# Optimization experiments

Hardware: AMD Instinct MI355X
Metric: run time of the kernel (lower is better)

Reference implementation:

```python
import jax, jax.numpy as jnp
import numpy as np

B, T, C = 2, 2048, 1024
H, HS, RD = 16, 64, 64
KV_R, Q_R = 256, 384


def _rope_tables(T, dim):
    # standard RoPE angle tables, shape [T, dim]
    half = dim // 2
    inv_freq = 1.0 / (10000.0 ** (np.arange(0, half, dtype=np.float32) / half))
    t = np.arange(T, dtype=np.float32)
    ang = np.outer(t, inv_freq)  # [T, half]
    ang = np.concatenate([ang, ang], axis=-1)  # [T, dim]
    return jnp.asarray(np.cos(ang)), jnp.asarray(np.sin(ang))


def setup_inputs() -> dict:
    key = jax.random.key(0)
    ks = jax.random.split(key, 8)
    cos, sin = _rope_tables(T, RD)
    s = lambda fan_in: 1.0 / np.sqrt(fan_in)
    return {
        "x": jax.random.normal(ks[0], (B, T, C), jnp.float32),
        "cos": cos,
        "sin": sin,
        "W_kv_down": jax.random.normal(ks[1], (C, KV_R), jnp.float32) * s(C),
        "W_kv_up": jax.random.normal(ks[2], (KV_R, H * HS), jnp.float32) * s(KV_R),
        "W_k_rope": jax.random.normal(ks[3], (KV_R, H * RD), jnp.float32) * s(KV_R),
        "W_q_down": jax.random.normal(ks[4], (C, Q_R), jnp.float32) * s(C),
        "W_q_up": jax.random.normal(ks[5], (Q_R, H * HS), jnp.float32) * s(Q_R),
        "W_q_rope": jax.random.normal(ks[6], (Q_R, H * RD), jnp.float32) * s(Q_R),
        "W_out": jax.random.normal(ks[7], (H * HS, C), jnp.float32) * s(H * HS),
    }


def _apply_rope(x, cos, sin):
    # x: [B,H,T,D]; cos/sin: [T,D] broadcast
    d = x.shape[-1]
    x1, x2 = x[..., : d // 2], x[..., d // 2 :]
    rotated = jnp.concatenate([-x2, x1], axis=-1)
    return x * cos + rotated * sin


def reference(x, cos, sin, W_kv_down, W_kv_up, W_k_rope, W_q_down, W_q_up, W_q_rope, W_out):
    Bx, Tx, Cx = x.shape
    to_heads = lambda z, d: jnp.swapaxes(z.reshape(Bx, Tx, H, d), 1, 2)  # [B,H,T,d]

    latent_kv = x @ W_kv_down                      # [B,T,KV_R]
    kv_up = latent_kv @ W_kv_up                    # [B,T,H*HS]
    v = to_heads(kv_up, HS)
    k_content = to_heads(kv_up, HS)                # same projection used for k and v
    k_rope = _apply_rope(to_heads(latent_kv @ W_k_rope, RD), cos[:Tx], sin[:Tx])

    latent_q = x @ W_q_down                        # [B,T,Q_R]
    q_content = to_heads(latent_q @ W_q_up, HS)
    q_rope = _apply_rope(to_heads(latent_q @ W_q_rope, RD), cos[:Tx], sin[:Tx])

    q = jnp.concatenate([q_content, q_rope], axis=-1)  # [B,H,T,HS+RD]
    k = jnp.concatenate([k_content, k_rope], axis=-1)

    att = jnp.einsum("bhqd,bhkd->bhqk", q, k) * (HS ** -0.5)
    causal = jnp.tril(jnp.ones((Tx, Tx), bool))
    att = jnp.where(causal, att, -jnp.inf)
    att = jax.nn.softmax(att, axis=-1)             # dropout is eval-mode identity
    y = jnp.einsum("bhqk,bhkd->bhqd", att, v)      # [B,H,T,HS]
    y = jnp.swapaxes(y, 1, 2).reshape(Bx, Tx, H * HS)
    return y @ W_out
```

## Files before the change

### kernel.cpp

```cpp
#include <hip/hip_runtime.h>
#include <stdint.h>

typedef unsigned short u16;
typedef __bf16 bf16x8 __attribute__((ext_vector_type(8)));
typedef float f32x4 __attribute__((ext_vector_type(4)));

#define B_ 2
#define T_ 2048

__device__ __forceinline__ u16 f2b(float f) {
  unsigned u = __float_as_uint(f);
  u += 0x7fffu + ((u >> 16) & 1u);
  return (u16)(u >> 16);
}
__device__ __forceinline__ unsigned cvt_pk(float lo, float hi) {
  unsigned r;
  asm("v_cvt_pk_bf16_f32 %0, %1, %2" : "=v"(r) : "v"(lo), "v"(hi));
  return r;
}
__device__ __forceinline__ float ex2(float x) {
  float r;
  asm("v_exp_f32 %0, %1" : "=v"(r) : "v"(x));
  return r;
}

using gu32 = __attribute__((address_space(1))) const unsigned int;
using lu32 = __attribute__((address_space(3))) unsigned int;
__device__ __forceinline__ void gl_lds16(const u16* g, u16* l) {
  __builtin_amdgcn_global_load_lds((gu32*)g, (lu32*)l, 16, 0, 0);
}

struct TJob { const float* src; u16* dst; int K, N, ldt, row_off, blk0; };
struct TJobs { TJob j[7]; };

__global__ __launch_bounds__(256) void prep_kernel(const float* __restrict__ x,
                                                   u16* __restrict__ xb, TJobs jobs) {
  int bid = blockIdx.x;
  int tid = threadIdx.x;
  if (bid < 4096) {
    int i = (bid * 256 + tid) * 4;
    float4 v = *reinterpret_cast<const float4*>(x + i);
    union { u16 h[4]; unsigned long long ll; } pk;
    pk.h[0] = f2b(v.x); pk.h[1] = f2b(v.y); pk.h[2] = f2b(v.z); pk.h[3] = f2b(v.w);
    *reinterpret_cast<unsigned long long*>(xb + i) = pk.ll;
    return;
  }
  bid -= 4096;
  __shared__ float tile[32][33];
  int ji = 0;
  #pragma unroll
  for (int i = 6; i > 0; --i)
    if (bid >= jobs.j[i].blk0) { ji = i; break; }
  const TJob jb = jobs.j[ji];
  int local = bid - jb.blk0;
  int nb = jb.N >> 5;
  int n0 = (local % nb) * 32, k0 = (local / nb) * 32;
  int cx = tid & 31, ry = tid >> 5;
  #pragma unroll
  for (int i = 0; i < 4; i++)
    tile[ry + i * 8][cx] = jb.src[(size_t)(k0 + ry + i * 8) * jb.N + n0 + cx];
  __syncthreads();
  #pragma unroll
  for (int i = 0; i < 4; i++)
    jb.dst[(size_t)(jb.row_off + n0 + ry + i * 8) * jb.ldt + k0 + cx] =
        f2b(tile[cx][ry + i * 8]);
}

struct GJob { const u16* A; const u16* Bt; void* C; int lda, ldb, ldc, K, mode; };

__global__ __launch_bounds__(512) void gemm_bt8(GJob j0, GJob j1, int split,
                                                const float* __restrict__ cosT,
                                                const float* __restrict__ sinT) {
  __shared__ u16 As[2][128 * 64];
  __shared__ u16 Bs[2][128 * 64];
  const bool first = (int)blockIdx.x < split;
  const GJob jb = first ? j0 : j1;
  const int bx = blockIdx.x - (first ? 0 : split);
  const int tid = threadIdx.x;
  const int wave = tid >> 6, lane = tid & 63;
  const int wr = wave >> 1, wc = wave & 1;
  const int l15 = lane & 15, l4 = lane >> 4;
  const int m0 = blockIdx.y * 128, n0 = bx * 128;
  const int srow = lane >> 3;
  const int scol = ((lane & 7) ^ srow) * 8;

  f32x4 acc[2][4];
  const f32x4 fzero = {0.f, 0.f, 0.f, 0.f};
  #pragma unroll
  for (int m = 0; m < 2; m++)
    #pragma unroll
    for (int n = 0; n < 4; n++)
      acc[m][n] = fzero;

  const u16* gA = jb.A  + (size_t)(m0 + wave * 16 + srow) * jb.lda + scol;
  const u16* gB = jb.Bt + (size_t)(n0 + wave * 16 + srow) * jb.ldb + scol;

  auto stage = [&](int buf, int k0) {
    gl_lds16(gA + k0,                      &As[buf][(wave * 16) * 64]);
    gl_lds16(gA + (size_t)8 * jb.lda + k0, &As[buf][(wave * 16 + 8) * 64]);
    gl_lds16(gB + k0,                      &Bs[buf][(wave * 16) * 64]);
    gl_lds16(gB + (size_t)8 * jb.ldb + k0, &Bs[buf][(wave * 16 + 8) * 64]);
  };

  stage(0, 0);
  int buf = 0;
  const int K = jb.K;
  for (int k0 = 0; k0 < K; k0 += 64) {
    asm volatile("s_waitcnt vmcnt(0)" ::: "memory");
    __builtin_amdgcn_s_barrier();
    if (k0 + 64 < K) stage(buf ^ 1, k0 + 64);
    bf16x8 af[2][2], bfr[4][2];
    #pragma unroll
    for (int m = 0; m < 2; m++) {
      const int row = wr * 32 + m * 16 + l15;
      const int xm = (row & 7) * 8;
      af[m][0] = *reinterpret_cast<const bf16x8*>(&As[buf][row * 64 + ((l4 * 8) ^ xm)]);
      af[m][1] = *reinterpret_cast<const bf16x8*>(&As[buf][row * 64 + ((32 + l4 * 8) ^ xm)]);
    }
    #pragma unroll
    for (int n = 0; n < 4; n++) {
      const int row = wc * 64 + n * 16 + l15;
      const int xm = (row & 7) * 8;
      bfr[n][0] = *reinterpret_cast<const bf16x8*>(&Bs[buf][row * 64 + ((l4 * 8) ^ xm)]);
      bfr[n][1] = *reinterpret_cast<const bf16x8*>(&Bs[buf][row * 64 + ((32 + l4 * 8) ^ xm)]);
    }
    #pragma unroll
    for (int m = 0; m < 2; m++)
      #pragma unroll
      for (int n = 0; n < 4; n++) {
        acc[m][n] = __builtin_amdgcn_mfma_f32_16x16x32_bf16(af[m][0], bfr[n][0], acc[m][n], 0, 0, 0);
        acc[m][n] = __builtin_amdgcn_mfma_f32_16x16x32_bf16(af[m][1], bfr[n][1], acc[m][n], 0, 0, 0);
      }
    buf ^= 1;
  }

  const int row_base = m0 + wr * 32 + l4 * 4;
  const int col_base = n0 + wc * 64 + l15;
  const int mode = jb.mode;
  const int ldc = jb.ldc;

  if (mode == 1) {
    float* Cf = (float*)jb.C;
    #pragma unroll
    for (int m = 0; m < 2; m++)
      #pragma unroll
      for (int n = 0; n < 4; n++)
        #pragma unroll
        for (int r = 0; r < 4; r++)
          Cf[(size_t)(row_base + m * 16 + r) * ldc + col_base + n * 16] = acc[m][n][r];
    return;
  }

  if (mode >= 2 && (n0 + wc * 64) >= 1024) {
    #pragma unroll
    for (int m = 0; m < 2; m++)
      #pragma unroll
      for (int r = 0; r < 4; r++) {
        int t = (row_base + m * 16 + r) & (T_ - 1);
        const float* cp = cosT + t * 64 + l15;
        const float* sp = sinT + t * 64 + l15;
        float c0 = cp[0], c16 = cp[16], c32 = cp[32], c48 = cp[48];
        float s0 = sp[0], s16 = sp[16], s32 = sp[32], s48 = sp[48];
        float x0 = acc[m][0][r], x1 = acc[m][1][r];
        float x2 = acc[m][2][r], x3 = acc[m][3][r];
        acc[m][0][r] = x0 * c0 - x2 * s0;
        acc[m][1][r] = x1 * c16 - x3 * s16;
        acc[m][2][r] = x2 * c32 + x0 * s32;
        acc[m][3][r] = x3 * c48 + x1 * s48;
      }
  }

  u16* Cb = (u16*)jb.C;
  #pragma unroll
  for (int m = 0; m < 2; m++)
    #pragma unroll
    for (int n = 0; n < 4; n++)
      #pragma unroll
      for (int r = 0; r < 4; r++)
        Cb[(size_t)(row_base + m * 16 + r) * ldc + col_base + n * 16] = f2b(acc[m][n][r]);
}

__global__ __launch_bounds__(256) void vtrans_kernel(const u16* __restrict__ kvo,
                                                     u16* __restrict__ vt) {
  __shared__ u16 tile[64][72];
  const int tid = threadIdx.x;
  const int cb = blockIdx.x * 64;
  const int rb = blockIdx.y * 64;
  const int b = rb >> 11, t0 = rb & 2047;
  const int rr = tid >> 3;
  const int c8 = (tid & 7) * 8;
  #pragma unroll
  for (int i = 0; i < 2; i++) {
    int r = i * 32 + rr;
    uint4 v = *reinterpret_cast<const uint4*>(kvo + (size_t)(rb + r) * 2048 + cb + c8);
    *reinterpret_cast<uint4*>(&tile[r][c8]) = v;
  }
  __syncthreads();
  #pragma unroll
  for (int i = 0; i < 2; i++) {
    int c = i * 32 + rr;
    int r8 = c8;
    union { u16 h[8]; uint4 v; } pk;
    #pragma unroll
    for (int j = 0; j < 8; j++) pk.h[j] = tile[r8 + j][c];
    *reinterpret_cast<uint4*>(&vt[(size_t)(b * 1024 + cb + c) * 2048 + t0 + r8]) = pk.v;
  }
}

__global__ __launch_bounds__(512) void attn_kernel(const u16* __restrict__ qo,
                                                   const u16* __restrict__ kvo,
                                                   const u16* __restrict__ vtg,
                                                   u16* __restrict__ yb) {
  __shared__ u16 K_lds[2][64 * 128];
  __shared__ u16 V_lds[2][64 * 64];
  __shared__ u16 P_lds[8][16][72];
  const int tid = threadIdx.x;
  const int wave = tid >> 6, lane = tid & 63;
  const int l15 = lane & 15, l4 = lane >> 4;
  const int bid = blockIdx.x;
  const int bh = bid & 31;
  const int qi = 15 - (bid >> 5);
  const int b = bh >> 4, h = bh & 15;
  const int q0 = qi * 128;
  const int qrow = q0 + wave * 16 + l15;

  const u16* qb = qo + (size_t)(b * T_ + qrow) * 2048 + h * 64;
  bf16x8 qf[4];
  qf[0] = *reinterpret_cast<const bf16x8*>(qb + l4 * 8);
  qf[1] = *reinterpret_cast<const bf16x8*>(qb + 32 + l4 * 8);
  qf[2] = *reinterpret_cast<const bf16x8*>(qb + 1024 + l4 * 8);
  qf[3] = *reinterpret_cast<const bf16x8*>(qb + 1056 + l4 * 8);

  const u16* Kbase = kvo + (size_t)(b * T_) * 2048 + h * 64;
  const u16* Vbase = vtg + (size_t)(b * 1024 + h * 64) * 2048;

  const int krow_i = lane >> 4;
  const int kc2 = (lane & 15) * 16;
  const int vrow_i = lane >> 3;
  const int vc2 = (lane & 7) * 16;

  auto stage = [&](int buf, int kv0) {
    #pragma unroll
    for (int j = 0; j < 2; j++) {
      int row = wave * 8 + j * 4 + krow_i;
      int c2x = kc2 ^ ((row & 7) << 4);
      int cu = c2x >> 1;
      const u16* src = Kbase + (size_t)(kv0 + row) * 2048 + (cu < 64 ? cu : 960 + cu);
      gl_lds16(src, &K_lds[buf][(wave * 8 + j * 4) * 128]);
    }
    {
      int row = wave * 8 + vrow_i;
      int c2x = vc2 ^ ((row & 7) << 4);
      const u16* src = Vbase + (size_t)row * 2048 + kv0 + (c2x >> 1);
      gl_lds16(src, &V_lds[buf][(wave * 8) * 64]);
    }
  };

  const f32x4 fzero = {0.f, 0.f, 0.f, 0.f};
  f32x4 oT[4];
  #pragma unroll
  for (int f = 0; f < 4; f++) oT[f] = fzero;
  float m_run = -1e30f, l_run = 0.f;

  const float SCALE2 = 0.125f * 1.44269504f;
  const int nt = qi * 2 + 2;
  const int t_diag = qi * 2 + (wave >> 2);

  stage(0, 0);
  int buf = 0;

  for (int t = 0; t < nt; t++) {
    const int kv0 = t * 64;
    asm volatile("s_waitcnt vmcnt(0)" ::: "memory");
    __builtin_amdgcn_s_barrier();
    if (t + 1 < nt) stage(buf ^ 1, kv0 + 64);

    if (t <= t_diag) {
      const char* Kb = (const char*)&K_lds[buf][0];
      const char* Vb = (const char*)&V_lds[buf][0];

      f32x4 sT[4];
      #pragma unroll
      for (int c = 0; c < 4; c++) sT[c] = fzero;
      #pragma unroll
      for (int c = 0; c < 4; c++) {
        const int krow = c * 16 + l15;
        const int kxm = (krow & 7) << 4;
        #pragma unroll
        for (int s = 0; s < 4; s++) {
          bf16x8 kf = *reinterpret_cast<const bf16x8*>(
              Kb + krow * 256 + ((s * 64 + l4 * 16) ^ kxm));
          sT[c] = __builtin_amdgcn_mfma_f32_16x16x32_bf16(kf, qf[s], sT[c], 0, 0, 0);
        }
      }

      const bool diag = (t == t_diag);
      float p[4][4];
      float mx = -1e30f;
      #pragma unroll
      for (int c = 0; c < 4; c++)
        #pragma unroll
        for (int r = 0; r < 4; r++) {
          float s = sT[c][r] * SCALE2;
          if (diag) {
            int kv = kv0 + c * 16 + l4 * 4 + r;
            if (kv > qrow) s = -1e30f;
          }
          p[c][r] = s;
          mx = fmaxf(mx, s);
        }
      mx = fmaxf(mx, __shfl_xor(mx, 16));
      mx = fmaxf(mx, __shfl_xor(mx, 32));
      if (__any(mx > m_run + 11.5f)) {
        float m_new = fmaxf(m_run, mx);
        float corr = ex2(m_run - m_new);
        l_run *= corr;
        #pragma unroll
        for (int f = 0; f < 4; f++) oT[f] *= corr;
        m_run = m_new;
      }
      float rsum = 0.f;
      #pragma unroll
      for (int c = 0; c < 4; c++)
        #pragma unroll
        for (int r = 0; r < 4; r++) {
          float pe = ex2(p[c][r] - m_run);
          p[c][r] = pe;
          rsum += pe;
        }
      rsum += __shfl_xor(rsum, 16);
      rsum += __shfl_xor(rsum, 32);
      l_run += rsum;

      #pragma unroll
      for (int c = 0; c < 4; c++) {
        uint2 pk2;
        pk2.x = cvt_pk(p[c][0], p[c][1]);
        pk2.y = cvt_pk(p[c][2], p[c][3]);
        *reinterpret_cast<uint2*>(&P_lds[wave][l15][c * 16 + l4 * 4]) = pk2;
      }
      bf16x8 pb0 = *reinterpret_cast<const bf16x8*>(&P_lds[wave][l15][l4 * 8]);
      bf16x8 pb1 = *reinterpret_cast<const bf16x8*>(&P_lds[wave][l15][32 + l4 * 8]);

      #pragma unroll
      for (int f = 0; f < 4; f++) {
        const int vrow = f * 16 + l15;
        const int vxm = (vrow & 7) << 4;
        bf16x8 v0 = *reinterpret_cast<const bf16x8*>(Vb + vrow * 128 + ((l4 * 16) ^ vxm));
        bf16x8 v1 = *reinterpret_cast<const bf16x8*>(Vb + vrow * 128 + ((64 + l4 * 16) ^ vxm));
        oT[f] = __builtin_amdgcn_mfma_f32_16x16x32_bf16(v0, pb0, oT[f], 0, 0, 0);
        oT[f] = __builtin_amdgcn_mfma_f32_16x16x32_bf16(v1, pb1, oT[f], 0, 0, 0);
      }
    }

    buf ^= 1;
  }

  const float inv = 1.f / l_run;
  #pragma unroll
  for (int f = 0; f < 4; f++) {
    uint2 pk2;
    pk2.x = cvt_pk(oT[f][0] * inv, oT[f][1] * inv);
    pk2.y = cvt_pk(oT[f][2] * inv, oT[f][3] * inv);
    *reinterpret_cast<uint2*>(
        &yb[(size_t)(b * T_ + qrow) * 1024 + h * 64 + f * 16 + l4 * 4]) = pk2;
  }
}

extern "C" void kernel_launch(void* const* d_in, const int* in_sizes, int n_in,
                              void* d_out, int out_size, void* d_ws, size_t ws_size,
                              hipStream_t stream) {
  const float* x         = (const float*)d_in[0];
  const float* cosT      = (const float*)d_in[1];
  const float* sinT      = (const float*)d_in[2];
  const float* W_kv_down = (const float*)d_in[3];
  const float* W_kv_up   = (const float*)d_in[4];
  const float* W_k_rope  = (const float*)d_in[5];
  const float* W_q_down  = (const float*)d_in[6];
  const float* W_q_up    = (const float*)d_in[7];
  const float* W_q_rope  = (const float*)d_in[8];
  const float* W_out     = (const float*)d_in[9];
  float* out = (float*)d_out;
  char* ws = (char*)d_ws;

  u16* xb    = (u16*)(ws + 0);
  u16* lat   = (u16*)(ws + 8388608);
  u16* WdT   = (u16*)(ws + 13631488);
  u16* WkvT  = (u16*)(ws + 14942208);
  u16* WqT   = (u16*)(ws + 15990784);
  u16* WoutT = (u16*)(ws + 17563648);
  u16* kvo   = (u16*)(ws + 19660800);
  u16* qo    = (u16*)(ws + 36438016);
  u16* VT    = (u16*)(ws + 53215232);
  u16* yb    = (u16*)(ws + 0);

  TJobs jobs;
  jobs.j[0] = {W_kv_down, WdT,   1024, 256,  1024, 0,    0};
  jobs.j[1] = {W_q_down,  WdT,   1024, 384,  1024, 256,  256};
  jobs.j[2] = {W_kv_up,   WkvT,  256,  1024, 256,  0,    640};
  jobs.j[3] = {W_k_rope,  WkvT,  256,  1024, 256,  1024, 896};
  jobs.j[4] = {W_q_up,    WqT,   384,  1024, 384,  0,    1152};
  jobs.j[5] = {W_q_rope,  WqT,   384,  1024, 384,  1024, 1536};
  jobs.j[6] = {W_out,     WoutT, 1024, 1024, 1024, 0,    1920};
  prep_kernel<<<7040, 256, 0, stream>>>(x, xb, jobs);

  GJob g1 = {xb, WdT, lat, 1024, 1024, 640, 1024, 0};
  gemm_bt8<<<dim3(5, 32), 512, 0, stream>>>(g1, g1, 5, nullptr, nullptr);

  GJob g2 = {lat,       WkvT, kvo, 640, 256, 2048, 256, 2};
  GJob g3 = {lat + 256, WqT,  qo,  640, 384, 2048, 384, 3};
  gemm_bt8<<<dim3(32, 32), 512, 0, stream>>>(g2, g3, 16, cosT, sinT);

  vtrans_kernel<<<dim3(16, 64), 256, 0, stream>>>(kvo, VT);

  attn_kernel<<<512, 512, 0, stream>>>(qo, kvo, VT, yb);

  GJob g4 = {yb, WoutT, out, 1024, 1024, 1024, 1024, 1};
  gemm_bt8<<<dim3(8, 32), 512, 0, stream>>>(g4, g4, 8, nullptr, nullptr);
}
```

Before: 215.7 us.

## Feed P to PV MFMA from registers and use 64-row tiles for small GEMMs

In attention, the softmax probabilities are packed to bf16 and fed directly as the B operand of 16x16x16 bf16 MFMAs through inline asm. This drops the per-wave P round trip through shared memory, since the accumulator layout of QK^T matches the operand layout of the K=16 MFMA. V is now read as four 8-byte fragments instead of two 16-byte ones. Separately, the GEMM becomes a template over M-tile size, and the down-projection and output GEMMs use 64-row tiles to double the block count for better CU occupancy. The cost is more MFMA instructions of half the K depth and less reuse per block.

```diff
diff --git a/kernel.cpp b/kernel.cpp
--- a/kernel.cpp
+++ b/kernel.cpp
@@ -22,6 +22,10 @@
   float r;
   asm("v_exp_f32 %0, %1" : "=v"(r) : "v"(x));
   return r;
+}
+__device__ __forceinline__ void mfma16(f32x4& acc, uint2 a, uint2 b) {
+  asm volatile("v_mfma_f32_16x16x16_bf16 %0, %1, %2, %0"
+               : "+v"(acc) : "v"(a), "v"(b));
 }
 
 using gu32 = __attribute__((address_space(1))) const unsigned int;
@@ -68,10 +72,12 @@
 
 struct GJob { const u16* A; const u16* Bt; void* C; int lda, ldb, ldc, K, mode; };
 
-__global__ __launch_bounds__(512) void gemm_bt8(GJob j0, GJob j1, int split,
-                                                const float* __restrict__ cosT,
-                                                const float* __restrict__ sinT) {
-  __shared__ u16 As[2][128 * 64];
+template<int ID, int MT>
+__global__ __launch_bounds__(512) void gemm_k(GJob j0, GJob j1, int split,
+                                              const float* __restrict__ cosT,
+                                              const float* __restrict__ sinT) {
+  constexpr int MR = MT / 64;
+  __shared__ u16 As[2][MT * 64];
   __shared__ u16 Bs[2][128 * 64];
   const bool first = (int)blockIdx.x < split;
   const GJob jb = first ? j0 : j1;
@@ -80,24 +86,28 @@
   const int wave = tid >> 6, lane = tid & 63;
   const int wr = wave >> 1, wc = wave & 1;
   const int l15 = lane & 15, l4 = lane >> 4;
-  const int m0 = blockIdx.y * 128, n0 = bx * 128;
+  const int m0 = blockIdx.y * MT, n0 = bx * 128;
   const int srow = lane >> 3;
   const int scol = ((lane & 7) ^ srow) * 8;
 
-  f32x4 acc[2][4];
+  f32x4 acc[MR][4];
   const f32x4 fzero = {0.f, 0.f, 0.f, 0.f};
   #pragma unroll
-  for (int m = 0; m < 2; m++)
+  for (int m = 0; m < MR; m++)
     #pragma unroll
     for (int n = 0; n < 4; n++)
       acc[m][n] = fzero;
 
-  const u16* gA = jb.A  + (size_t)(m0 + wave * 16 + srow) * jb.lda + scol;
+  const u16* gA = jb.A + (size_t)(m0 + (MT == 128 ? wave * 16 : wave * 8) + srow) * jb.lda + scol;
   const u16* gB = jb.Bt + (size_t)(n0 + wave * 16 + srow) * jb.ldb + scol;
 
   auto stage = [&](int buf, int k0) {
-    gl_lds16(gA + k0,                      &As[buf][(wave * 16) * 64]);
-    gl_lds16(gA + (size_t)8 * jb.lda + k0, &As[buf][(wave * 16 + 8) * 64]);
+    if constexpr (MT == 128) {
+      gl_lds16(gA + k0,                      &As[buf][(wave * 16) * 64]);
+      gl_lds16(gA + (size_t)8 * jb.lda + k0, &As[buf][(wave * 16 + 8) * 64]);
+    } else {
+      gl_lds16(gA + k0, &As[buf][(wave * 8) * 64]);
+    }
     gl_lds16(gB + k0,                      &Bs[buf][(wave * 16) * 64]);
     gl_lds16(gB + (size_t)8 * jb.ldb + k0, &Bs[buf][(wave * 16 + 8) * 64]);
   };
@@ -109,10 +119,10 @@
     asm volatile("s_waitcnt vmcnt(0)" ::: "memory");
     __builtin_amdgcn_s_barrier();
     if (k0 + 64 < K) stage(buf ^ 1, k0 + 64);
-    bf16x8 af[2][2], bfr[4][2];
-    #pragma unroll
-    for (int m = 0; m < 2; m++) {
-      const int row = wr * 32 + m * 16 + l15;
+    bf16x8 af[MR][2], bfr[4][2];
+    #pragma unroll
+    for (int m = 0; m < MR; m++) {
+      const int row = wr * (MT / 4) + m * 16 + l15;
       const int xm = (row & 7) * 8;
       af[m][0] = *reinterpret_cast<const bf16x8*>(&As[buf][row * 64 + ((l4 * 8) ^ xm)]);
       af[m][1] = *reinterpret_cast<const bf16x8*>(&As[buf][row * 64 + ((32 + l4 * 8) ^ xm)]);
@@ -125,7 +135,7 @@
       bfr[n][1] = *reinterpret_cast<const bf16x8*>(&Bs[buf][row * 64 + ((32 + l4 * 8) ^ xm)]);
     }
     #pragma unroll
-    for (int m = 0; m < 2; m++)
+    for (int m = 0; m < MR; m++)
       #pragma unroll
       for (int n = 0; n < 4; n++) {
         acc[m][n] = __builtin_amdgcn_mfma_f32_16x16x32_bf16(af[m][0], bfr[n][0], acc[m][n], 0, 0, 0);
@@ -134,7 +144,7 @@
     buf ^= 1;
   }
 
-  const int row_base = m0 + wr * 32 + l4 * 4;
+  const int row_base = m0 + wr * (MT / 4) + l4 * 4;
   const int col_base = n0 + wc * 64 + l15;
   const int mode = jb.mode;
   const int ldc = jb.ldc;
@@ -142,7 +152,7 @@
   if (mode == 1) {
     float* Cf = (float*)jb.C;
     #pragma unroll
-    for (int m = 0; m < 2; m++)
+    for (int m = 0; m < MR; m++)
       #pragma unroll
       for (int n = 0; n < 4; n++)
         #pragma unroll
@@ -153,7 +163,7 @@
 
   if (mode >= 2 && (n0 + wc * 64) >= 1024) {
     #pragma unroll
-    for (int m = 0; m < 2; m++)
+    for (int m = 0; m < MR; m++)
       #pragma unroll
       for (int r = 0; r < 4; r++) {
         int t = (row_base + m * 16 + r) & (T_ - 1);
@@ -172,7 +182,7 @@
 
   u16* Cb = (u16*)jb.C;
   #pragma unroll
-  for (int m = 0; m < 2; m++)
+  for (int m = 0; m < MR; m++)
     #pragma unroll
     for (int n = 0; n < 4; n++)
       #pragma unroll
@@ -213,7 +223,6 @@
                                                    u16* __restrict__ yb) {
   __shared__ u16 K_lds[2][64 * 128];
   __shared__ u16 V_lds[2][64 * 64];
-  __shared__ u16 P_lds[8][16][72];
   const int tid = threadIdx.x;
   const int wave = tid >> 6, lane = tid & 63;
   const int l15 = lane & 15, l4 = lane >> 4;
@@ -332,24 +341,23 @@
       rsum += __shfl_xor(rsum, 32);
       l_run += rsum;
 
+      uint2 pc[4];
       #pragma unroll
       for (int c = 0; c < 4; c++) {
-        uint2 pk2;
-        pk2.x = cvt_pk(p[c][0], p[c][1]);
-        pk2.y = cvt_pk(p[c][2], p[c][3]);
-        *reinterpret_cast<uint2*>(&P_lds[wave][l15][c * 16 + l4 * 4]) = pk2;
-      }
-      bf16x8 pb0 = *reinterpret_cast<const bf16x8*>(&P_lds[wave][l15][l4 * 8]);
-      bf16x8 pb1 = *reinterpret_cast<const bf16x8*>(&P_lds[wave][l15][32 + l4 * 8]);
+        pc[c].x = cvt_pk(p[c][0], p[c][1]);
+        pc[c].y = cvt_pk(p[c][2], p[c][3]);
+      }
 
       #pragma unroll
       for (int f = 0; f < 4; f++) {
         const int vrow = f * 16 + l15;
         const int vxm = (vrow & 7) << 4;
-        bf16x8 v0 = *reinterpret_cast<const bf16x8*>(Vb + vrow * 128 + ((l4 * 16) ^ vxm));
-        bf16x8 v1 = *reinterpret_cast<const bf16x8*>(Vb + vrow * 128 + ((64 + l4 * 16) ^ vxm));
-        oT[f] = __builtin_amdgcn_mfma_f32_16x16x32_bf16(v0, pb0, oT[f], 0, 0, 0);
-        oT[f] = __builtin_amdgcn_mfma_f32_16x16x32_bf16(v1, pb1, oT[f], 0, 0, 0);
+        #pragma unroll
+        for (int c = 0; c < 4; c++) {
+          uint2 va = *reinterpret_cast<const uint2*>(
+              Vb + vrow * 128 + ((c * 32 + l4 * 8) ^ vxm));
+          mfma16(oT[f], va, pc[c]);
+        }
       }
     }
 
@@ -405,16 +413,16 @@
   prep_kernel<<<7040, 256, 0, stream>>>(x, xb, jobs);
 
   GJob g1 = {xb, WdT, lat, 1024, 1024, 640, 1024, 0};
-  gemm_bt8<<<dim3(5, 32), 512, 0, stream>>>(g1, g1, 5, nullptr, nullptr);
+  gemm_k<0, 64><<<dim3(5, 64), 512, 0, stream>>>(g1, g1, 5, nullptr, nullptr);
 
   GJob g2 = {lat,       WkvT, kvo, 640, 256, 2048, 256, 2};
   GJob g3 = {lat + 256, WqT,  qo,  640, 384, 2048, 384, 3};
-  gemm_bt8<<<dim3(32, 32), 512, 0, stream>>>(g2, g3, 16, cosT, sinT);
+  gemm_k<1, 128><<<dim3(32, 32), 512, 0, stream>>>(g2, g3, 16, cosT, sinT);
 
   vtrans_kernel<<<dim3(16, 64), 256, 0, stream>>>(kvo, VT);
 
   attn_kernel<<<512, 512, 0, stream>>>(qo, kvo, VT, yb);
 
   GJob g4 = {yb, WoutT, out, 1024, 1024, 1024, 1024, 1};
-  gemm_bt8<<<dim3(8, 32), 512, 0, stream>>>(g4, g4, 8, nullptr, nullptr);
-}
+  gemm_k<2, 64><<<dim3(8, 64), 512, 0, stream>>>(g4, g4, 8, nullptr, nullptr);
+}
```

New measurement: 213.8 us. No clear change (-0.9%).
